# Kernel tuning notes

Hardware: AMD Instinct MI355X
Metric: run time of the kernel (lower is better)

The kernel has to match this reference:

```python
import jax, jax.numpy as jnp
import numpy as np

TOP_K = 2
NUM_EXPERTS = 16
CAPACITY = 512          # >> avg load (128/expert) so no token is ever dropped in practice
FP8_MAX = 448.0         # float8_e4m3fn max representable magnitude


def _fp8_quant(v, axes):
    """Simulated fp8 e4m3 dynamic quantization: amax scaling + clipping.
    Returns (quantized values, scale with keepdims)."""
    s = jnp.clip(jnp.max(jnp.abs(v), axis=axes, keepdims=True) / FP8_MAX, 1e-12, None)
    return jnp.clip(v / s, -FP8_MAX, FP8_MAX), s


def setup_inputs() -> dict:
    key = jax.random.key(0)
    k0, k1, k2, k3 = jax.random.split(key, 4)
    T, H, I, E = 1024, 2048, 1408, NUM_EXPERTS
    x = jax.random.normal(k0, (T, H), jnp.float32)
    router_logits = jax.random.normal(k1, (T, E), jnp.float32)
    w13_weight = jax.random.normal(k2, (E, 2 * I, H), jnp.float32) * 0.02
    w2_weight = jax.random.normal(k3, (E, H, I), jnp.float32) * 0.02
    return {"x": x, "router_logits": router_logits,
            "w13_weight": w13_weight, "w2_weight": w2_weight}


def reference(x, router_logits, w13_weight, w2_weight):
    T, H = x.shape
    E, K, C = NUM_EXPERTS, TOP_K, CAPACITY
    I = w2_weight.shape[2]

    # --- routing: softmax -> top-k -> renormalize ---
    probs = jax.nn.softmax(router_logits, axis=-1)               # [T, E]
    topw, topi = jax.lax.top_k(probs, K)                          # [T, K]
    topw = topw / jnp.sum(topw, axis=-1, keepdims=True)

    # --- dispatch: flatten (token, k) rows, rank within expert ---
    rid = topi.reshape(-1)                                        # [T*K] expert id per row
    rtok = jnp.arange(T * K) // K                                 # source token per row
    order = jnp.argsort(rid)                                      # jax sort is stable
    counts = jnp.bincount(rid, length=E)
    offsets = jnp.concatenate([jnp.zeros(1, counts.dtype), jnp.cumsum(counts)[:-1]])
    pos_sorted = jnp.arange(T * K) - offsets[rid[order]]
    pos = jnp.zeros(T * K, jnp.int32).at[order].set(pos_sorted.astype(jnp.int32))
    valid = pos < C                                               # capacity is generous: no drops
    posc = jnp.minimum(pos, C - 1)

    xrows = x[rtok] * valid[:, None].astype(x.dtype)              # [T*K, H]
    xbuf = jnp.zeros((E, C, H), x.dtype).at[rid, posc].add(xrows)  # [E, C, H]

    # --- grouped GEMM 1 (gate+up), fp8 w8a8: per-expert weight scale, per-token act scale ---
    w13q, sw13 = _fp8_quant(w13_weight, (1, 2))                   # sw13 [E,1,1]
    xq, sa1 = _fp8_quant(xbuf, -1)                                # sa1  [E,C,1]
    h = jnp.einsum('ech,efh->ecf', xq, w13q) * (sa1 * sw13)       # [E, C, 2I]

    # --- silu_and_mul ---
    gate, up = h[..., :I], h[..., I:]
    act = jax.nn.silu(gate) * up                                  # [E, C, I]

    # --- grouped GEMM 2 (down) ---
    w2q, sw2 = _fp8_quant(w2_weight, (1, 2))                      # sw2 [E,1,1]
    aq, sa2 = _fp8_quant(act, -1)                                 # sa2 [E,C,1]
    ybuf = jnp.einsum('eci,ehi->ech', aq, w2q) * (sa2 * sw2)      # [E, C, H]

    # --- combine: gather back and weight by router probs ---
    yrows = ybuf[rid, posc] * valid[:, None].astype(x.dtype)      # [T*K, H]
    out = jnp.einsum('tkh,tk->th', yrows.reshape(T, K, H), topw)  # [T, H]
    return out
```

## Files before the change

### kernel.cpp

```cpp
#include <hip/hip_runtime.h>
#include <hip/hip_bf16.h>
#include <math.h>

#define NEXP 16
#define CAP  512
#define TTOK 1024
#define HDIM 2048
#define IDIM 1408

typedef float fx4 __attribute__((ext_vector_type(4)));
typedef short short8 __attribute__((ext_vector_type(8)));
typedef unsigned int u32;
typedef unsigned long long u64;

__device__ __forceinline__ unsigned short f2bf(float f) {
    u32 u = __float_as_uint(f);
    u += 0x7FFFu + ((u >> 16) & 1u);
    return (unsigned short)(u >> 16);
}
__device__ __forceinline__ float bf2f(unsigned short h) {
    return __uint_as_float(((u32)h) << 16);
}
__device__ __forceinline__ u64 pack4bf(fx4 f) {
    u32 lo = (u32)f2bf(f.x) | ((u32)f2bf(f.y) << 16);
    u32 hi = (u32)f2bf(f.z) | ((u32)f2bf(f.w) << 16);
    return (u64)lo | ((u64)hi << 32);
}

__global__ void router_kernel(const float* __restrict__ logits,
                              int* __restrict__ topi, float* __restrict__ topw,
                              int* __restrict__ cnt1) {
    int t = blockIdx.x * blockDim.x + threadIdx.x;
    if (t >= TTOK) return;
    const float* l = logits + t * NEXP;
    float b0 = -INFINITY, b1 = -INFINITY; int i0 = 0, i1 = 0;
    for (int e = 0; e < NEXP; ++e) {
        float v = l[e];
        if (v > b0) { b1 = b0; i1 = i0; b0 = v; i0 = e; }
        else if (v > b1) { b1 = v; i1 = e; }
    }
    float w0 = 1.f / (1.f + expf(b1 - b0));
    topi[t*2]   = i0; topi[t*2+1] = i1;
    topw[t*2]   = w0; topw[t*2+1] = 1.f - w0;
    atomicAdd(&cnt1[i0], 1);
    atomicAdd(&cnt1[i1], 1);
}

__global__ void scan_kernel(const int* __restrict__ cnt1, int* __restrict__ base) {
    if (threadIdx.x == 0 && blockIdx.x == 0) {
        int s = 0;
        for (int e = 0; e < NEXP; ++e) {
            base[e] = s;
            int c = cnt1[e]; if (c > CAP) c = CAP;
            s += c;
        }
        base[NEXP] = s;
    }
}

__global__ void assign_kernel(const int* __restrict__ topi, const int* __restrict__ base,
                              int* __restrict__ cnt2,
                              int* __restrict__ slot_token, int* __restrict__ slot_of) {
    int t = blockIdx.x * blockDim.x + threadIdx.x;
    if (t >= TTOK) return;
    for (int k = 0; k < 2; ++k) {
        int e = topi[t*2+k];
        int p = atomicAdd(&cnt2[e], 1);
        if (p < CAP) {
            int s = base[e] + p;
            slot_token[s] = t;
            slot_of[t*2+k] = s;
        } else {
            slot_of[t*2+k] = -1;
        }
    }
}

#define LDA 40

template<int NDIM, int KDIM, bool GATHER>
__global__ __launch_bounds__(256) void gemm_bt_kernel(
    const float* __restrict__ Af32,
    const unsigned short* __restrict__ Abf16,
    const float* __restrict__ W,
    unsigned short* __restrict__ Cout,
    const int* __restrict__ slot_token,
    const int* __restrict__ base)
{
    const int e = blockIdx.z;
    const int n0 = base[e];
    const int rows = base[e+1] - n0;
    const int rtile = blockIdx.y * 128;
    if (rtile >= rows) return;
    const int col0 = blockIdx.x * 64;

    __shared__ unsigned short sA[2][128 * LDA];
    __shared__ unsigned short sB[2][64 * LDA];

    const int tid = threadIdx.x;
    const int lane = tid & 63;
    const int wv = tid >> 6;
    const int lr = lane & 15;
    const int quad = lane >> 4;

    fx4 acc[2][4];
    #pragma unroll
    for (int i = 0; i < 2; ++i)
        #pragma unroll
        for (int j = 0; j < 4; ++j) acc[i][j] = (fx4)0.f;

    const int bg = tid & 7, bc = tid >> 3;
    const int ag = tid & 7, ar = tid >> 3;
    const int ag2 = tid & 3, ar2 = tid >> 2;

    int tok[4];
    if (GATHER) {
        #pragma unroll
        for (int p = 0; p < 4; ++p) {
            int grow = rtile + ar + p*32;
            tok[p] = (grow < rows) ? slot_token[n0 + grow] : -1;
        }
    } else {
        #pragma unroll
        for (int p = 0; p < 2; ++p) {
            int grow = rtile + ar2 + p*64;
            tok[p] = (grow < rows) ? (n0 + grow) : -1;
        }
    }

    const float* Wp = W + ((size_t)e * NDIM + col0) * KDIM;

    fx4 pa[4], pb[2];

    auto prefetch = [&](int k0) {
        #pragma unroll
        for (int p = 0; p < 2; ++p)
            pb[p] = *(const fx4*)(Wp + (size_t)(bc + p*32) * KDIM + k0 + bg*4);
        if (GATHER) {
            #pragma unroll
            for (int p = 0; p < 4; ++p)
                pa[p] = (tok[p] >= 0)
                    ? *(const fx4*)(Af32 + (size_t)tok[p]*KDIM + k0 + ag*4)
                    : (fx4)0.f;
        } else {
            #pragma unroll
            for (int p = 0; p < 2; ++p)
                pa[p] = (tok[p] >= 0)
                    ? *(const fx4*)(Abf16 + (size_t)tok[p]*KDIM + k0 + ag2*8)
                    : (fx4)0.f;
        }
    };
    auto stage = [&](int buf) {
        #pragma unroll
        for (int p = 0; p < 2; ++p)
            *(u64*)&sB[buf][(bc + p*32)*LDA + bg*4] = pack4bf(pb[p]);
        if (GATHER) {
            #pragma unroll
            for (int p = 0; p < 4; ++p)
                *(u64*)&sA[buf][(ar + p*32)*LDA + ag*4] = pack4bf(pa[p]);
        } else {
            #pragma unroll
            for (int p = 0; p < 2; ++p)
                *(fx4*)&sA[buf][(ar2 + p*64)*LDA + ag2*8] = pa[p];
        }
    };

    prefetch(0);
    stage(0);
    __syncthreads();

    const int KT = KDIM / 32;
    for (int kt = 0; kt < KT; ++kt) {
        const int cur = kt & 1;
        if (kt + 1 < KT) prefetch((kt + 1) * 32);

        short8 af[2], bfr[4];
        #pragma unroll
        for (int mi = 0; mi < 2; ++mi)
            af[mi] = *(const short8*)&sA[cur][(wv*32 + mi*16 + lr)*LDA + quad*8];
        #pragma unroll
        for (int ni = 0; ni < 4; ++ni)
            bfr[ni] = *(const short8*)&sB[cur][(ni*16 + lr)*LDA + quad*8];
        #pragma unroll
        for (int mi = 0; mi < 2; ++mi)
            #pragma unroll
            for (int ni = 0; ni < 4; ++ni)
                acc[mi][ni] = __builtin_amdgcn_mfma_f32_16x16x32_bf16(
                    af[mi], bfr[ni], acc[mi][ni], 0, 0, 0);

        if (kt + 1 < KT) {
            stage(1 - cur);
            __syncthreads();
        }
    }

    #pragma unroll
    for (int mi = 0; mi < 2; ++mi) {
        #pragma unroll
        for (int r = 0; r < 4; ++r) {
            int grow = rtile + wv*32 + mi*16 + quad*4 + r;
            if (grow < rows) {
                size_t orow = (size_t)(n0 + grow) * NDIM;
                #pragma unroll
                for (int ni = 0; ni < 4; ++ni) {
                    int gcol = col0 + ni*16 + lr;
                    Cout[orow + gcol] = f2bf(acc[mi][ni][r]);
                }
            }
        }
    }
}

__global__ void silu_kernel(const unsigned short* __restrict__ h,
                            unsigned short* __restrict__ act,
                            const int* __restrict__ base) {
    const int R = base[NEXP];
    int idx = blockIdx.x * blockDim.x + threadIdx.x;
    int row = idx / (IDIM/8);
    int j   = idx % (IDIM/8);
    if (row >= R) return;
    const unsigned short* g = h + (size_t)row * (2*IDIM) + j*8;
    const unsigned short* u = g + IDIM;
    unsigned short go[8], uo[8], ao[8];
    *(fx4*)go = *(const fx4*)g;
    *(fx4*)uo = *(const fx4*)u;
    #pragma unroll
    for (int i = 0; i < 8; ++i) {
        float gv = bf2f(go[i]), uv = bf2f(uo[i]);
        float s = gv / (1.f + __expf(-gv));
        ao[i] = f2bf(s * uv);
    }
    *(fx4*)&act[(size_t)row*IDIM + j*8] = *(fx4*)ao;
}

__global__ void combine_kernel(const unsigned short* __restrict__ ybuf,
                               const int* __restrict__ slot_of,
                               const float* __restrict__ topw,
                               float* __restrict__ out) {
    int t = blockIdx.x;
    int c = threadIdx.x * 8;
    int s0 = slot_of[t*2], s1 = slot_of[t*2+1];
    float w0 = topw[t*2], w1 = topw[t*2+1];
    float res[8];
    #pragma unroll
    for (int i = 0; i < 8; ++i) res[i] = 0.f;
    if (s0 >= 0) {
        unsigned short y[8];
        *(fx4*)y = *(const fx4*)(ybuf + (size_t)s0*HDIM + c);
        #pragma unroll
        for (int i = 0; i < 8; ++i) res[i] += w0 * bf2f(y[i]);
    }
    if (s1 >= 0) {
        unsigned short y[8];
        *(fx4*)y = *(const fx4*)(ybuf + (size_t)s1*HDIM + c);
        #pragma unroll
        for (int i = 0; i < 8; ++i) res[i] += w1 * bf2f(y[i]);
    }
    float* o = out + (size_t)t*HDIM + c;
    *(fx4*)o       = *(fx4*)res;
    *(fx4*)(o + 4) = *(fx4*)(res + 4);
}

extern "C" void kernel_launch(void* const* d_in, const int* in_sizes, int n_in,
                              void* d_out, int out_size, void* d_ws, size_t ws_size,
                              hipStream_t stream) {
    const float* x      = (const float*)d_in[0];
    const float* logits = (const float*)d_in[1];
    const float* w13    = (const float*)d_in[2];
    const float* w2     = (const float*)d_in[3];
    float* out = (float*)d_out;

    char* ws = (char*)d_ws;
    size_t off = 0;
    auto alloc = [&](size_t bytes) -> void* {
        void* p = ws + off;
        off += (bytes + 255) & ~(size_t)255;
        return p;
    };
    int*   topi       = (int*)  alloc(TTOK*2*sizeof(int));
    float* topw       = (float*)alloc(TTOK*2*sizeof(float));
    int*   cnt1       = (int*)  alloc(NEXP*sizeof(int));
    int*   cnt2       = (int*)  alloc(NEXP*sizeof(int));
    int*   base       = (int*)  alloc((NEXP+1)*sizeof(int));
    int*   slot_token = (int*)  alloc(TTOK*2*sizeof(int));
    int*   slot_of    = (int*)  alloc(TTOK*2*sizeof(int));
    unsigned short* h    = (unsigned short*)alloc((size_t)TTOK*2 * (2*IDIM) * 2);
    unsigned short* act  = (unsigned short*)alloc((size_t)TTOK*2 * IDIM * 2);
    unsigned short* ybuf = (unsigned short*)alloc((size_t)TTOK*2 * HDIM * 2);

    hipMemsetAsync(cnt1, 0, NEXP*sizeof(int), stream);
    hipMemsetAsync(cnt2, 0, NEXP*sizeof(int), stream);

    router_kernel<<<dim3((TTOK+255)/256), 256, 0, stream>>>(logits, topi, topw, cnt1);
    scan_kernel<<<1, 64, 0, stream>>>(cnt1, base);
    assign_kernel<<<dim3((TTOK+255)/256), 256, 0, stream>>>(topi, base, cnt2, slot_token, slot_of);

    gemm_bt_kernel<2*IDIM, HDIM, true>
        <<<dim3(2*IDIM/64, CAP/128, NEXP), 256, 0, stream>>>(
            x, nullptr, w13, h, slot_token, base);

    silu_kernel<<<dim3((TTOK*2*(IDIM/8) + 255)/256), 256, 0, stream>>>(h, act, base);

    gemm_bt_kernel<HDIM, IDIM, false>
        <<<dim3(HDIM/64, CAP/128, NEXP), 256, 0, stream>>>(
            nullptr, act, w2, ybuf, slot_token, base);

    combine_kernel<<<dim3(TTOK), 256, 0, stream>>>(ybuf, slot_of, topw, out);
}
```

Measured before the change: 758.5 us.

## Split-K both grouped GEMMs into fp32 partials and deepen register prefetch

Splits the K dimension of both expert GEMMs in two, doubling the grid so more workgroups run concurrently, and writes fp32 partial sums that the silu and combine kernels add together. The register prefetch is also made two stages deep so global loads run further ahead of the MFMA work. The cost is extra global traffic from fp32 partial buffers at twice the size, which the elementwise kernels now read, plus more register use for the deeper prefetch.

```diff
diff --git a/kernel.cpp b/kernel.cpp
--- a/kernel.cpp
+++ b/kernel.cpp
@@ -7,6 +7,7 @@
 #define TTOK 1024
 #define HDIM 2048
 #define IDIM 1408
+#define MAXR (TTOK*2)
 
 typedef float fx4 __attribute__((ext_vector_type(4)));
 typedef short short8 __attribute__((ext_vector_type(8)));
@@ -78,21 +79,23 @@
 
 #define LDA 40
 
-template<int NDIM, int KDIM, bool GATHER>
+template<int NDIM, int KDIM, int SK, bool GATHER>
 __global__ __launch_bounds__(256) void gemm_bt_kernel(
     const float* __restrict__ Af32,
     const unsigned short* __restrict__ Abf16,
     const float* __restrict__ W,
-    unsigned short* __restrict__ Cout,
+    float* __restrict__ Cpart,
     const int* __restrict__ slot_token,
     const int* __restrict__ base)
 {
     const int e = blockIdx.z;
     const int n0 = base[e];
     const int rows = base[e+1] - n0;
-    const int rtile = blockIdx.y * 128;
+    const int ks = blockIdx.y % SK;
+    const int rtile = (blockIdx.y / SK) * 128;
     if (rtile >= rows) return;
     const int col0 = blockIdx.x * 64;
+    const int kbase = ks * (KDIM / SK);
 
     __shared__ unsigned short sA[2][128 * LDA];
     __shared__ unsigned short sB[2][64 * LDA];
@@ -128,51 +131,52 @@
         }
     }
 
-    const float* Wp = W + ((size_t)e * NDIM + col0) * KDIM;
-
-    fx4 pa[4], pb[2];
-
-    auto prefetch = [&](int k0) {
+    const float* Wp = W + ((size_t)e * NDIM + col0) * KDIM + kbase;
+
+    fx4 pa[2][4], pb[2][2];
+
+    auto prefetch = [&](int slot, int k0) {
         #pragma unroll
         for (int p = 0; p < 2; ++p)
-            pb[p] = *(const fx4*)(Wp + (size_t)(bc + p*32) * KDIM + k0 + bg*4);
+            pb[slot][p] = *(const fx4*)(Wp + (size_t)(bc + p*32) * KDIM + k0 + bg*4);
         if (GATHER) {
             #pragma unroll
             for (int p = 0; p < 4; ++p)
-                pa[p] = (tok[p] >= 0)
-                    ? *(const fx4*)(Af32 + (size_t)tok[p]*KDIM + k0 + ag*4)
+                pa[slot][p] = (tok[p] >= 0)
+                    ? *(const fx4*)(Af32 + (size_t)tok[p]*KDIM + kbase + k0 + ag*4)
                     : (fx4)0.f;
         } else {
             #pragma unroll
             for (int p = 0; p < 2; ++p)
-                pa[p] = (tok[p] >= 0)
-                    ? *(const fx4*)(Abf16 + (size_t)tok[p]*KDIM + k0 + ag2*8)
+                pa[slot][p] = (tok[p] >= 0)
+                    ? *(const fx4*)(Abf16 + (size_t)tok[p]*KDIM + kbase + k0 + ag2*8)
                     : (fx4)0.f;
         }
     };
-    auto stage = [&](int buf) {
+    auto stage = [&](int buf, int slot) {
         #pragma unroll
         for (int p = 0; p < 2; ++p)
-            *(u64*)&sB[buf][(bc + p*32)*LDA + bg*4] = pack4bf(pb[p]);
+            *(u64*)&sB[buf][(bc + p*32)*LDA + bg*4] = pack4bf(pb[slot][p]);
         if (GATHER) {
             #pragma unroll
             for (int p = 0; p < 4; ++p)
-                *(u64*)&sA[buf][(ar + p*32)*LDA + ag*4] = pack4bf(pa[p]);
+                *(u64*)&sA[buf][(ar + p*32)*LDA + ag*4] = pack4bf(pa[slot][p]);
         } else {
             #pragma unroll
             for (int p = 0; p < 2; ++p)
-                *(fx4*)&sA[buf][(ar2 + p*64)*LDA + ag2*8] = pa[p];
+                *(fx4*)&sA[buf][(ar2 + p*64)*LDA + ag2*8] = pa[slot][p];
         }
     };
 
-    prefetch(0);
-    stage(0);
+    const int KT = (KDIM / SK) / 32;
+    prefetch(0, 0);
+    stage(0, 0);
+    if (KT > 1) prefetch(1, 32);
     __syncthreads();
 
-    const int KT = KDIM / 32;
     for (int kt = 0; kt < KT; ++kt) {
         const int cur = kt & 1;
-        if (kt + 1 < KT) prefetch((kt + 1) * 32);
+        if (kt + 2 < KT) prefetch(cur, (kt + 2) * 32);
 
         short8 af[2], bfr[4];
         #pragma unroll
@@ -189,11 +193,12 @@
                     af[mi], bfr[ni], acc[mi][ni], 0, 0, 0);
 
         if (kt + 1 < KT) {
-            stage(1 - cur);
+            stage(1 - cur, 1 - cur);
             __syncthreads();
         }
     }
 
+    float* Cp = Cpart + (size_t)ks * MAXR * NDIM;
     #pragma unroll
     for (int mi = 0; mi < 2; ++mi) {
         #pragma unroll
@@ -204,14 +209,14 @@
                 #pragma unroll
                 for (int ni = 0; ni < 4; ++ni) {
                     int gcol = col0 + ni*16 + lr;
-                    Cout[orow + gcol] = f2bf(acc[mi][ni][r]);
+                    Cp[orow + gcol] = acc[mi][ni][r];
                 }
             }
         }
     }
 }
 
-__global__ void silu_kernel(const unsigned short* __restrict__ h,
+__global__ void silu_kernel(const float* __restrict__ h,
                             unsigned short* __restrict__ act,
                             const int* __restrict__ base) {
     const int R = base[NEXP];
@@ -219,21 +224,24 @@
     int row = idx / (IDIM/8);
     int j   = idx % (IDIM/8);
     if (row >= R) return;
-    const unsigned short* g = h + (size_t)row * (2*IDIM) + j*8;
-    const unsigned short* u = g + IDIM;
-    unsigned short go[8], uo[8], ao[8];
-    *(fx4*)go = *(const fx4*)g;
-    *(fx4*)uo = *(const fx4*)u;
+    const float* g0 = h + (size_t)row * (2*IDIM) + j*8;
+    const float* g1 = g0 + (size_t)MAXR * (2*IDIM);
+    float gate[8], up[8];
+    *(fx4*)&gate[0] = *(const fx4*)g0        + *(const fx4*)g1;
+    *(fx4*)&gate[4] = *(const fx4*)(g0+4)    + *(const fx4*)(g1+4);
+    *(fx4*)&up[0]   = *(const fx4*)(g0+IDIM)   + *(const fx4*)(g1+IDIM);
+    *(fx4*)&up[4]   = *(const fx4*)(g0+IDIM+4) + *(const fx4*)(g1+IDIM+4);
+    unsigned short ao[8];
     #pragma unroll
     for (int i = 0; i < 8; ++i) {
-        float gv = bf2f(go[i]), uv = bf2f(uo[i]);
+        float gv = gate[i];
         float s = gv / (1.f + __expf(-gv));
-        ao[i] = f2bf(s * uv);
+        ao[i] = f2bf(s * up[i]);
     }
     *(fx4*)&act[(size_t)row*IDIM + j*8] = *(fx4*)ao;
 }
 
-__global__ void combine_kernel(const unsigned short* __restrict__ ybuf,
+__global__ void combine_kernel(const float* __restrict__ ypart,
                                const int* __restrict__ slot_of,
                                const float* __restrict__ topw,
                                float* __restrict__ out) {
@@ -241,20 +249,21 @@
     int c = threadIdx.x * 8;
     int s0 = slot_of[t*2], s1 = slot_of[t*2+1];
     float w0 = topw[t*2], w1 = topw[t*2+1];
+    const float* y1b = ypart + (size_t)MAXR * HDIM;
     float res[8];
     #pragma unroll
     for (int i = 0; i < 8; ++i) res[i] = 0.f;
     if (s0 >= 0) {
-        unsigned short y[8];
-        *(fx4*)y = *(const fx4*)(ybuf + (size_t)s0*HDIM + c);
-        #pragma unroll
-        for (int i = 0; i < 8; ++i) res[i] += w0 * bf2f(y[i]);
+        const float* p0 = ypart + (size_t)s0*HDIM + c;
+        const float* p1 = y1b   + (size_t)s0*HDIM + c;
+        #pragma unroll
+        for (int i = 0; i < 8; ++i) res[i] += w0 * (p0[i] + p1[i]);
     }
     if (s1 >= 0) {
-        unsigned short y[8];
-        *(fx4*)y = *(const fx4*)(ybuf + (size_t)s1*HDIM + c);
-        #pragma unroll
-        for (int i = 0; i < 8; ++i) res[i] += w1 * bf2f(y[i]);
+        const float* p0 = ypart + (size_t)s1*HDIM + c;
+        const float* p1 = y1b   + (size_t)s1*HDIM + c;
+        #pragma unroll
+        for (int i = 0; i < 8; ++i) res[i] += w1 * (p0[i] + p1[i]);
     }
     float* o = out + (size_t)t*HDIM + c;
     *(fx4*)o       = *(fx4*)res;
@@ -284,9 +293,9 @@
     int*   base       = (int*)  alloc((NEXP+1)*sizeof(int));
     int*   slot_token = (int*)  alloc(TTOK*2*sizeof(int));
     int*   slot_of    = (int*)  alloc(TTOK*2*sizeof(int));
-    unsigned short* h    = (unsigned short*)alloc((size_t)TTOK*2 * (2*IDIM) * 2);
-    unsigned short* act  = (unsigned short*)alloc((size_t)TTOK*2 * IDIM * 2);
-    unsigned short* ybuf = (unsigned short*)alloc((size_t)TTOK*2 * HDIM * 2);
+    float* hpart = (float*)alloc((size_t)2 * MAXR * (2*IDIM) * sizeof(float));
+    unsigned short* act = (unsigned short*)alloc((size_t)MAXR * IDIM * 2);
+    float* ypart = (float*)alloc((size_t)2 * MAXR * HDIM * sizeof(float));
 
     hipMemsetAsync(cnt1, 0, NEXP*sizeof(int), stream);
     hipMemsetAsync(cnt2, 0, NEXP*sizeof(int), stream);
@@ -295,15 +304,15 @@
     scan_kernel<<<1, 64, 0, stream>>>(cnt1, base);
     assign_kernel<<<dim3((TTOK+255)/256), 256, 0, stream>>>(topi, base, cnt2, slot_token, slot_of);
 
-    gemm_bt_kernel<2*IDIM, HDIM, true>
-        <<<dim3(2*IDIM/64, CAP/128, NEXP), 256, 0, stream>>>(
-            x, nullptr, w13, h, slot_token, base);
-
-    silu_kernel<<<dim3((TTOK*2*(IDIM/8) + 255)/256), 256, 0, stream>>>(h, act, base);
-
-    gemm_bt_kernel<HDIM, IDIM, false>
-        <<<dim3(HDIM/64, CAP/128, NEXP), 256, 0, stream>>>(
-            nullptr, act, w2, ybuf, slot_token, base);
-
-    combine_kernel<<<dim3(TTOK), 256, 0, stream>>>(ybuf, slot_of, topw, out);
-}
+    gemm_bt_kernel<2*IDIM, HDIM, 2, true>
+        <<<dim3(2*IDIM/64, (CAP/128)*2, NEXP), 256, 0, stream>>>(
+            x, nullptr, w13, hpart, slot_token, base);
+
+    silu_kernel<<<dim3((TTOK*2*(IDIM/8) + 255)/256), 256, 0, stream>>>(hpart, act, base);
+
+    gemm_bt_kernel<HDIM, IDIM, 2, false>
+        <<<dim3(HDIM/64, (CAP/128)*2, NEXP), 256, 0, stream>>>(
+            nullptr, act, w2, ypart, slot_token, base);
+
+    combine_kernel<<<dim3(TTOK), 256, 0, stream>>>(ypart, slot_of, topw, out);
+}
```

Result: faster. 730.9 us (-3.6%).
